# Optimization experiments

Measured on AMD Instinct MI355X. Metric: run time of the kernel, lower is better.

The kernel has to match this reference:

```python
import jax, jax.numpy as jnp
import numpy as np

N, B, F = 204800, 4096, 256

def setup_inputs() -> dict:
    key = jax.random.key(0)
    ks = jax.random.split(key, 8)
    s = 1.0 / np.sqrt(F)
    return {
        'node_feats': jax.random.normal(ks[0], (N, F), jnp.float32),
        'g_feats': jax.random.normal(ks[1], (B, F), jnp.float32),
        'segment_ids': jnp.sort(jax.random.randint(ks[2], (N,), 0, B, jnp.int32)),
        'W_logit': jax.random.normal(ks[3], (1, 2 * F), jnp.float32) * (1.0 / np.sqrt(2 * F)),
        'b_logit': jnp.zeros((1,), jnp.float32),
        'W_proj': jax.random.normal(ks[4], (F, F), jnp.float32) * s,
        'b_proj': jnp.zeros((F,), jnp.float32),
        'W_ih': jax.random.normal(ks[5], (3 * F, F), jnp.float32) * s,
        'W_hh': jax.random.normal(ks[6], (3 * F, F), jnp.float32) * s,
        'b_ih': jnp.zeros((3 * F,), jnp.float32),
        'b_hh': jnp.zeros((3 * F,), jnp.float32),
    }

def reference(node_feats, g_feats, segment_ids, W_logit, b_logit, W_proj, b_proj, W_ih, W_hh, b_ih, b_hh):
    num_graphs = g_feats.shape[0]
    # logits: Linear(2F -> 1) on [broadcast(relu(g_feats)), node_feats], then LeakyReLU(0.01)
    ctx_nodes = jax.nn.relu(g_feats)[segment_ids]                      # [N, F]
    z = jnp.concatenate([ctx_nodes, node_feats], axis=1) @ W_logit.T + b_logit  # [N, 1]
    z = jax.nn.leaky_relu(z, negative_slope=0.01)
    # per-graph segment softmax over nodes
    zmax = jax.ops.segment_max(z, segment_ids, num_segments=num_graphs)
    z_exp = jnp.exp(z - zmax[segment_ids])
    denom = jax.ops.segment_sum(z_exp, segment_ids, num_segments=num_graphs)
    a = z_exp / denom[segment_ids]                                     # [N, 1]
    # project nodes (Dropout is identity at eval) and weighted segment sum
    hv = node_feats @ W_proj.T + b_proj                                # [N, F]
    g_repr = jax.ops.segment_sum(a * hv, segment_ids, num_segments=num_graphs)  # [B, F]
    context = jax.nn.elu(g_repr)
    # PyTorch GRUCell: input=context, hidden=g_feats
    gi = context @ W_ih.T + b_ih                                       # [B, 3F]
    gh = g_feats @ W_hh.T + b_hh
    i_r, i_z, i_n = jnp.split(gi, 3, axis=1)
    h_r, h_z, h_n = jnp.split(gh, 3, axis=1)
    r = jax.nn.sigmoid(i_r + h_r)
    zg = jax.nn.sigmoid(i_z + h_z)
    n = jnp.tanh(i_n + r * h_n)
    return (1.0 - zg) * n + zg * g_feats
```

## Files before the change

kernel.cpp:

```cpp
#include <hip/hip_runtime.h>

#define NN 204800
#define BB 4096
#define FF 256
#define CAP 64

typedef unsigned short u16;
typedef unsigned int u32;
typedef short bf16x8 __attribute__((ext_vector_type(8)));
typedef float f32x4  __attribute__((ext_vector_type(4)));

__device__ __forceinline__ u16 rne_bf16(float f){
    union { u32 v; float f; } t; t.f = f;
    u32 lsb = (t.v >> 16) & 1u;
    t.v += 0x7fffu + lsb;
    return (u16)(t.v >> 16);
}

__global__ void k_prep(const float* __restrict__ gfe, const float* __restrict__ Wp,
                       const float* __restrict__ Wih, const float* __restrict__ Whh,
                       const int* __restrict__ seg, int* __restrict__ start,
                       u16* __restrict__ gfe_b, u16* __restrict__ Wp_b,
                       u16* __restrict__ Wih_b, u16* __restrict__ Whh_b){
    int i = blockIdx.x * 256 + threadIdx.x;
    if (i <= BB){
        int lo = 0, hi = NN;
        while (lo < hi){ int mid = (lo + hi) >> 1; if (seg[mid] < i) lo = mid + 1; else hi = mid; }
        start[i] = lo;
    }
    const int n_gfe = BB * FF;
    const int n_wp  = FF * FF;
    const int n_w3  = 3 * FF * FF;
    int j = i;
    if (j < n_gfe){ gfe_b[j] = rne_bf16(gfe[j]); return; }
    j -= n_gfe;
    if (j < n_wp){ Wp_b[j] = rne_bf16(Wp[j]); return; }
    j -= n_wp;
    if (j < n_w3){ Wih_b[j] = rne_bf16(Wih[j]); return; }
    j -= n_w3;
    if (j < n_w3){ Whh_b[j] = rne_bf16(Whh[j]); return; }
}
#define PREP_TOTAL (BB*FF + FF*FF + 2*3*FF*FF)

__global__ void k_ctx_logit(const float* __restrict__ gfe, const float* __restrict__ Wl,
                            const float* __restrict__ bl, float* __restrict__ c){
    int wave = threadIdx.x >> 6, lane = threadIdx.x & 63;
    int g = blockIdx.x * 4 + wave;
    float4 gv = *(const float4*)(gfe + (size_t)g * FF + lane * 4);
    float4 wv = *(const float4*)(Wl + lane * 4);
    float sum = wv.x * fmaxf(gv.x, 0.f) + wv.y * fmaxf(gv.y, 0.f)
              + wv.z * fmaxf(gv.z, 0.f) + wv.w * fmaxf(gv.w, 0.f);
    #pragma unroll
    for (int o = 32; o; o >>= 1) sum += __shfl_xor(sum, o);
    if (lane == 0) c[g] = sum + bl[0];
}

__global__ __launch_bounds__(256) void k_attn(
        const float* __restrict__ x, const float* __restrict__ Wl,
        const float* __restrict__ c, const int* __restrict__ start,
        u16* __restrict__ s_b){
    __shared__ __align__(16) float xs[CAP][FF];
    __shared__ float zs[512];
    __shared__ float red[8];
    int g = blockIdx.x;
    int s0 = start[g], cnt = start[g + 1] - s0;
    int tid = threadIdx.x, wave = tid >> 6, lane = tid & 63;
    if (cnt == 0){
        s_b[(size_t)g * FF + tid] = 0;
        return;
    }
    float4 wv = *(const float4*)(Wl + FF + lane * 4);
    float cg = c[g];
    int i = wave;
    for (; i + 4 < cnt; i += 8){
        float4 xv0 = *(const float4*)(x + (size_t)(s0 + i) * FF + lane * 4);
        float4 xv1 = *(const float4*)(x + (size_t)(s0 + i + 4) * FF + lane * 4);
        if (i < CAP) *(float4*)(&xs[i][lane * 4]) = xv0;
        if (i + 4 < CAP) *(float4*)(&xs[i + 4][lane * 4]) = xv1;
        float d0 = xv0.x * wv.x + xv0.y * wv.y + xv0.z * wv.z + xv0.w * wv.w;
        float d1 = xv1.x * wv.x + xv1.y * wv.y + xv1.z * wv.z + xv1.w * wv.w;
        #pragma unroll
        for (int o = 32; o; o >>= 1){ d0 += __shfl_xor(d0, o); d1 += __shfl_xor(d1, o); }
        if (lane == 0){
            float t0 = cg + d0; zs[i] = t0 >= 0.f ? t0 : 0.01f * t0;
            float t1 = cg + d1; zs[i + 4] = t1 >= 0.f ? t1 : 0.01f * t1;
        }
    }
    for (; i < cnt; i += 4){
        float4 xv = *(const float4*)(x + (size_t)(s0 + i) * FF + lane * 4);
        if (i < CAP) *(float4*)(&xs[i][lane * 4]) = xv;
        float d = xv.x * wv.x + xv.y * wv.y + xv.z * wv.z + xv.w * wv.w;
        #pragma unroll
        for (int o = 32; o; o >>= 1) d += __shfl_xor(d, o);
        if (lane == 0){
            float t = cg + d; zs[i] = t >= 0.f ? t : 0.01f * t;
        }
    }
    __syncthreads();
    float mx = -3.4e38f;
    for (int k = tid; k < cnt; k += 256) mx = fmaxf(mx, zs[k]);
    #pragma unroll
    for (int o = 32; o; o >>= 1) mx = fmaxf(mx, __shfl_xor(mx, o));
    if (lane == 0) red[wave] = mx;
    __syncthreads();
    mx = fmaxf(fmaxf(red[0], red[1]), fmaxf(red[2], red[3]));
    float dsum = 0.f;
    for (int k = tid; k < cnt; k += 256){
        float e = expf(zs[k] - mx);
        zs[k] = e;
        dsum += e;
    }
    #pragma unroll
    for (int o = 32; o; o >>= 1) dsum += __shfl_xor(dsum, o);
    if (lane == 0) red[4 + wave] = dsum;
    __syncthreads();
    float inv = 1.f / (red[4] + red[5] + red[6] + red[7]);
    float acc = 0.f;
    int lim = cnt < CAP ? cnt : CAP;
    for (int k = 0; k < lim; k++) acc += zs[k] * xs[k][tid];
    for (int k = CAP; k < cnt; k++) acc += zs[k] * x[(size_t)(s0 + k) * FF + tid];
    s_b[(size_t)g * FF + tid] = rne_bf16(acc * inv);
}

__global__ __launch_bounds__(256) void k_proj_mfma(
        const u16* __restrict__ s_b, const u16* __restrict__ Wp_b,
        const float* __restrict__ bp, const int* __restrict__ gate,
        u16* __restrict__ ctx_b){
    int tid = threadIdx.x;
    int w = tid >> 6, l = tid & 63;
    int mn = l & 15, q = l >> 4;
    int m0 = blockIdx.x * 64 + w * 16;
    int f0 = blockIdx.y * 64;
    f32x4 acc[4] = {};
    const u16* arow = s_b + (size_t)(m0 + mn) * FF + q * 8;
    #pragma unroll
    for (int kb = 0; kb < 8; kb++){
        bf16x8 a = *(const bf16x8*)(arow + kb * 32);
        #pragma unroll
        for (int cc = 0; cc < 4; cc++){
            bf16x8 b = *(const bf16x8*)(Wp_b + (size_t)(f0 + cc * 16 + mn) * FF + kb * 32 + q * 8);
            acc[cc] = __builtin_amdgcn_mfma_f32_16x16x32_bf16(a, b, acc[cc], 0, 0, 0);
        }
    }
    #pragma unroll
    for (int cc = 0; cc < 4; cc++){
        int f = f0 + cc * 16 + mn;
        float bias = bp[f];
        #pragma unroll
        for (int r = 0; r < 4; r++){
            int g = m0 + q * 4 + r;
            float bs = (gate[g + 1] > gate[g]) ? 1.f : 0.f;
            float v = acc[cc][r] + bs * bias;
            v = v > 0.f ? v : expm1f(v);
            ctx_b[(size_t)g * FF + f] = rne_bf16(v);
        }
    }
}

__global__ __launch_bounds__(256) void k_gru_mfma(
        const u16* __restrict__ ctx_b, const u16* __restrict__ gfe_b,
        const u16* __restrict__ Wih_b, const u16* __restrict__ Whh_b,
        const float* __restrict__ bih, const float* __restrict__ bhh,
        const float* __restrict__ gfe, float* __restrict__ out){
    int tid = threadIdx.x;
    int w = tid >> 6, l = tid & 63;
    int mn = l & 15, q = l >> 4;
    int g0 = blockIdx.x * 64 + w * 16;
    int f0 = blockIdx.y * 64;
    f32x4 ai[3][4] = {};
    f32x4 ah[3][4] = {};
    const u16* ac_row = ctx_b + (size_t)(g0 + mn) * FF + q * 8;
    const u16* ag_row = gfe_b + (size_t)(g0 + mn) * FF + q * 8;
    #pragma unroll
    for (int kb = 0; kb < 8; kb++){
        bf16x8 a_c = *(const bf16x8*)(ac_row + kb * 32);
        bf16x8 a_g = *(const bf16x8*)(ag_row + kb * 32);
        #pragma unroll
        for (int s = 0; s < 3; s++){
            #pragma unroll
            for (int cc = 0; cc < 4; cc++){
                size_t woff = (size_t)(s * FF + f0 + cc * 16 + mn) * FF + kb * 32 + q * 8;
                bf16x8 bi = *(const bf16x8*)(Wih_b + woff);
                ai[s][cc] = __builtin_amdgcn_mfma_f32_16x16x32_bf16(a_c, bi, ai[s][cc], 0, 0, 0);
                bf16x8 bh = *(const bf16x8*)(Whh_b + woff);
                ah[s][cc] = __builtin_amdgcn_mfma_f32_16x16x32_bf16(a_g, bh, ah[s][cc], 0, 0, 0);
            }
        }
    }
    #pragma unroll
    for (int cc = 0; cc < 4; cc++){
        int f = f0 + cc * 16 + mn;
        float bir = bih[f], biz = bih[FF + f], bin_ = bih[2 * FF + f];
        float bhr = bhh[f], bhz = bhh[FF + f], bhn = bhh[2 * FF + f];
        #pragma unroll
        for (int r = 0; r < 4; r++){
            int g = g0 + q * 4 + r;
            float rg = 1.f / (1.f + expf(-(ai[0][cc][r] + bir + ah[0][cc][r] + bhr)));
            float zg = 1.f / (1.f + expf(-(ai[1][cc][r] + biz + ah[1][cc][r] + bhz)));
            float ng = tanhf(ai[2][cc][r] + bin_ + rg * (ah[2][cc][r] + bhn));
            float h = gfe[(size_t)g * FF + f];
            out[(size_t)g * FF + f] = (1.f - zg) * ng + zg * h;
        }
    }
}

extern "C" void kernel_launch(void* const* d_in, const int* in_sizes, int n_in,
                              void* d_out, int out_size, void* d_ws, size_t ws_size,
                              hipStream_t stream){
    const float* node = (const float*)d_in[0];
    const float* gfe  = (const float*)d_in[1];
    const int*   seg  = (const int*)d_in[2];
    const float* Wl   = (const float*)d_in[3];
    const float* bl   = (const float*)d_in[4];
    const float* Wp   = (const float*)d_in[5];
    const float* bp   = (const float*)d_in[6];
    const float* Wih  = (const float*)d_in[7];
    const float* Whh  = (const float*)d_in[8];
    const float* bih  = (const float*)d_in[9];
    const float* bhh  = (const float*)d_in[10];
    float* out = (float*)d_out;

    char* p = (char*)d_ws;
    auto alloc = [&](size_t bytes)->void*{
        void* r = (void*)p; p += (bytes + 255) & ~(size_t)255; return r;
    };
    int*   start = (int*)  alloc((BB + 1) * sizeof(int));
    float* c     = (float*)alloc(BB * sizeof(float));
    u16*   s_b   = (u16*)  alloc((size_t)BB * FF * sizeof(u16));
    u16*   ctx_b = (u16*)  alloc((size_t)BB * FF * sizeof(u16));
    u16*   gfe_b = (u16*)  alloc((size_t)BB * FF * sizeof(u16));
    u16*   Wp_b  = (u16*)  alloc((size_t)FF * FF * sizeof(u16));
    u16*   Wih_b = (u16*)  alloc((size_t)3 * FF * FF * sizeof(u16));
    u16*   Whh_b = (u16*)  alloc((size_t)3 * FF * FF * sizeof(u16));

    k_prep<<<(PREP_TOTAL + 255) / 256, 256, 0, stream>>>(gfe, Wp, Wih, Whh, seg, start,
                                                         gfe_b, Wp_b, Wih_b, Whh_b);
    k_ctx_logit<<<BB / 4, 256, 0, stream>>>(gfe, Wl, bl, c);
    k_attn<<<BB, 256, 0, stream>>>(node, Wl, c, start, s_b);
    k_proj_mfma<<<dim3(BB / 64, FF / 64), 256, 0, stream>>>(s_b, Wp_b, bp, start, ctx_b);
    k_gru_mfma<<<dim3(BB / 64, FF / 64), 256, 0, stream>>>(ctx_b, gfe_b, Wih_b, Whh_b,
                                                           bih, bhh, gfe, out);
}
```

Baseline: 385.5 us.

## Fuse context logit into attention, store staged rows as bf16, vectorize prep

```diff
diff --git a/kernel.cpp b/kernel.cpp
--- a/kernel.cpp
+++ b/kernel.cpp
@@ -3,7 +3,7 @@
 #define NN 204800
 #define BB 4096
 #define FF 256
-#define CAP 64
+#define CAP 72
 
 typedef unsigned short u16;
 typedef unsigned int u32;
@@ -15,6 +15,16 @@
     u32 lsb = (t.v >> 16) & 1u;
     t.v += 0x7fffu + lsb;
     return (u16)(t.v >> 16);
+}
+__device__ __forceinline__ float bf16_to_f(u16 h){
+    union { u32 v; float f; } t; t.v = (u32)h << 16; return t.f;
+}
+__device__ __forceinline__ void cvt4(const float* __restrict__ src, u16* __restrict__ dst){
+    float4 v = *(const float4*)src;
+    ushort4 h;
+    h.x = rne_bf16(v.x); h.y = rne_bf16(v.y);
+    h.z = rne_bf16(v.z); h.w = rne_bf16(v.w);
+    *(ushort4*)dst = h;
 }
 
 __global__ void k_prep(const float* __restrict__ gfe, const float* __restrict__ Wp,
@@ -31,37 +41,24 @@
     const int n_gfe = BB * FF;
     const int n_wp  = FF * FF;
     const int n_w3  = 3 * FF * FF;
-    int j = i;
-    if (j < n_gfe){ gfe_b[j] = rne_bf16(gfe[j]); return; }
+    int j = i * 4;
+    if (j < n_gfe){ cvt4(gfe + j, gfe_b + j); return; }
     j -= n_gfe;
-    if (j < n_wp){ Wp_b[j] = rne_bf16(Wp[j]); return; }
+    if (j < n_wp){ cvt4(Wp + j, Wp_b + j); return; }
     j -= n_wp;
-    if (j < n_w3){ Wih_b[j] = rne_bf16(Wih[j]); return; }
+    if (j < n_w3){ cvt4(Wih + j, Wih_b + j); return; }
     j -= n_w3;
-    if (j < n_w3){ Whh_b[j] = rne_bf16(Whh[j]); return; }
-}
-#define PREP_TOTAL (BB*FF + FF*FF + 2*3*FF*FF)
-
-__global__ void k_ctx_logit(const float* __restrict__ gfe, const float* __restrict__ Wl,
-                            const float* __restrict__ bl, float* __restrict__ c){
-    int wave = threadIdx.x >> 6, lane = threadIdx.x & 63;
-    int g = blockIdx.x * 4 + wave;
-    float4 gv = *(const float4*)(gfe + (size_t)g * FF + lane * 4);
-    float4 wv = *(const float4*)(Wl + lane * 4);
-    float sum = wv.x * fmaxf(gv.x, 0.f) + wv.y * fmaxf(gv.y, 0.f)
-              + wv.z * fmaxf(gv.z, 0.f) + wv.w * fmaxf(gv.w, 0.f);
-    #pragma unroll
-    for (int o = 32; o; o >>= 1) sum += __shfl_xor(sum, o);
-    if (lane == 0) c[g] = sum + bl[0];
-}
+    if (j < n_w3){ cvt4(Whh + j, Whh_b + j); return; }
+}
+#define PREP_V4 ((BB*FF + FF*FF + 2*3*FF*FF) / 4)
 
 __global__ __launch_bounds__(256) void k_attn(
         const float* __restrict__ x, const float* __restrict__ Wl,
-        const float* __restrict__ c, const int* __restrict__ start,
-        u16* __restrict__ s_b){
-    __shared__ __align__(16) float xs[CAP][FF];
+        const float* __restrict__ bl, const float* __restrict__ gfe,
+        const int* __restrict__ start, u16* __restrict__ s_b){
+    __shared__ __align__(16) u16 xs[CAP][FF];
     __shared__ float zs[512];
-    __shared__ float red[8];
+    __shared__ float red[16];
     int g = blockIdx.x;
     int s0 = start[g], cnt = start[g + 1] - s0;
     int tid = threadIdx.x, wave = tid >> 6, lane = tid & 63;
@@ -69,36 +66,61 @@
         s_b[(size_t)g * FF + tid] = 0;
         return;
     }
+    float p = Wl[tid] * fmaxf(gfe[(size_t)g * FF + tid], 0.f);
+    #pragma unroll
+    for (int o = 32; o; o >>= 1) p += __shfl_xor(p, o);
+    if (lane == 0) red[8 + wave] = p;
+    float blv = bl[0];
     float4 wv = *(const float4*)(Wl + FF + lane * 4);
-    float cg = c[g];
+
+    auto st_row = [&](int row, const float4& v){
+        ushort4 h;
+        h.x = rne_bf16(v.x); h.y = rne_bf16(v.y);
+        h.z = rne_bf16(v.z); h.w = rne_bf16(v.w);
+        *(ushort4*)(&xs[row][lane * 4]) = h;
+    };
+
     int i = wave;
-    for (; i + 4 < cnt; i += 8){
-        float4 xv0 = *(const float4*)(x + (size_t)(s0 + i) * FF + lane * 4);
-        float4 xv1 = *(const float4*)(x + (size_t)(s0 + i + 4) * FF + lane * 4);
-        if (i < CAP) *(float4*)(&xs[i][lane * 4]) = xv0;
-        if (i + 4 < CAP) *(float4*)(&xs[i + 4][lane * 4]) = xv1;
+    for (; i + 12 < cnt; i += 16){
+        const float* r0 = x + (size_t)(s0 + i) * FF + lane * 4;
+        float4 xv0 = *(const float4*)(r0);
+        float4 xv1 = *(const float4*)(r0 + 4 * FF);
+        float4 xv2 = *(const float4*)(r0 + 8 * FF);
+        float4 xv3 = *(const float4*)(r0 + 12 * FF);
         float d0 = xv0.x * wv.x + xv0.y * wv.y + xv0.z * wv.z + xv0.w * wv.w;
         float d1 = xv1.x * wv.x + xv1.y * wv.y + xv1.z * wv.z + xv1.w * wv.w;
-        #pragma unroll
-        for (int o = 32; o; o >>= 1){ d0 += __shfl_xor(d0, o); d1 += __shfl_xor(d1, o); }
+        float d2 = xv2.x * wv.x + xv2.y * wv.y + xv2.z * wv.z + xv2.w * wv.w;
+        float d3 = xv3.x * wv.x + xv3.y * wv.y + xv3.z * wv.z + xv3.w * wv.w;
+        #pragma unroll
+        for (int o = 32; o; o >>= 1){
+            d0 += __shfl_xor(d0, o); d1 += __shfl_xor(d1, o);
+            d2 += __shfl_xor(d2, o); d3 += __shfl_xor(d3, o);
+        }
+        if (i      < CAP) st_row(i,      xv0);
+        if (i + 4  < CAP) st_row(i + 4,  xv1);
+        if (i + 8  < CAP) st_row(i + 8,  xv2);
+        if (i + 12 < CAP) st_row(i + 12, xv3);
         if (lane == 0){
-            float t0 = cg + d0; zs[i] = t0 >= 0.f ? t0 : 0.01f * t0;
-            float t1 = cg + d1; zs[i + 4] = t1 >= 0.f ? t1 : 0.01f * t1;
+            zs[i] = d0; zs[i + 4] = d1; zs[i + 8] = d2; zs[i + 12] = d3;
         }
     }
     for (; i < cnt; i += 4){
         float4 xv = *(const float4*)(x + (size_t)(s0 + i) * FF + lane * 4);
-        if (i < CAP) *(float4*)(&xs[i][lane * 4]) = xv;
         float d = xv.x * wv.x + xv.y * wv.y + xv.z * wv.z + xv.w * wv.w;
         #pragma unroll
         for (int o = 32; o; o >>= 1) d += __shfl_xor(d, o);
-        if (lane == 0){
-            float t = cg + d; zs[i] = t >= 0.f ? t : 0.01f * t;
-        }
+        if (i < CAP) st_row(i, xv);
+        if (lane == 0) zs[i] = d;
     }
     __syncthreads();
+    float cg = red[8] + red[9] + red[10] + red[11] + blv;
     float mx = -3.4e38f;
-    for (int k = tid; k < cnt; k += 256) mx = fmaxf(mx, zs[k]);
+    for (int k = tid; k < cnt; k += 256){
+        float t = cg + zs[k];
+        t = t >= 0.f ? t : 0.01f * t;
+        zs[k] = t;
+        mx = fmaxf(mx, t);
+    }
     #pragma unroll
     for (int o = 32; o; o >>= 1) mx = fmaxf(mx, __shfl_xor(mx, o));
     if (lane == 0) red[wave] = mx;
@@ -117,7 +139,7 @@
     float inv = 1.f / (red[4] + red[5] + red[6] + red[7]);
     float acc = 0.f;
     int lim = cnt < CAP ? cnt : CAP;
-    for (int k = 0; k < lim; k++) acc += zs[k] * xs[k][tid];
+    for (int k = 0; k < lim; k++) acc += zs[k] * bf16_to_f(xs[k][tid]);
     for (int k = CAP; k < cnt; k++) acc += zs[k] * x[(size_t)(s0 + k) * FF + tid];
     s_b[(size_t)g * FF + tid] = rne_bf16(acc * inv);
 }
@@ -225,7 +247,6 @@
         void* r = (void*)p; p += (bytes + 255) & ~(size_t)255; return r;
     };
     int*   start = (int*)  alloc((BB + 1) * sizeof(int));
-    float* c     = (float*)alloc(BB * sizeof(float));
     u16*   s_b   = (u16*)  alloc((size_t)BB * FF * sizeof(u16));
     u16*   ctx_b = (u16*)  alloc((size_t)BB * FF * sizeof(u16));
     u16*   gfe_b = (u16*)  alloc((size_t)BB * FF * sizeof(u16));
@@ -233,10 +254,9 @@
     u16*   Wih_b = (u16*)  alloc((size_t)3 * FF * FF * sizeof(u16));
     u16*   Whh_b = (u16*)  alloc((size_t)3 * FF * FF * sizeof(u16));
 
-    k_prep<<<(PREP_TOTAL + 255) / 256, 256, 0, stream>>>(gfe, Wp, Wih, Whh, seg, start,
-                                                         gfe_b, Wp_b, Wih_b, Whh_b);
-    k_ctx_logit<<<BB / 4, 256, 0, stream>>>(gfe, Wl, bl, c);
-    k_attn<<<BB, 256, 0, stream>>>(node, Wl, c, start, s_b);
+    k_prep<<<(PREP_V4 + 255) / 256, 256, 0, stream>>>(gfe, Wp, Wih, Whh, seg, start,
+                                                      gfe_b, Wp_b, Wih_b, Whh_b);
+    k_attn<<<BB, 256, 0, stream>>>(node, Wl, bl, gfe, start, s_b);
     k_proj_mfma<<<dim3(BB / 64, FF / 64), 256, 0, stream>>>(s_b, Wp_b, bp, start, ctx_b);
     k_gru_mfma<<<dim3(BB / 64, FF / 64), 256, 0, stream>>>(ctx_b, gfe_b, Wih_b, Whh_b,
                                                            bih, bhh, gfe, out);
```

New measurement: 370.1 us. 1.04x faster.
